# Optimization experiments

Hardware: AMD Instinct MI355X
Metric: run time of the kernel (lower is better)

## Reference

```python
import jax, jax.numpy as jnp
import numpy as np

N_NODES = 50000
N_EDGES = 800000
N_GRAPHS = 128


def gcn_conv(x, row, col, W, b, num_nodes):
    # GCNConv: x' = D^-1/2 (A + I) D^-1/2 (x W) + b, with self-loops added.
    h = x @ W  # [N, out]
    # append self-loops
    sl = jnp.arange(num_nodes, dtype=row.dtype)
    r = jnp.concatenate([row, sl])
    c = jnp.concatenate([col, sl])
    deg = jax.ops.segment_sum(jnp.ones_like(r, dtype=h.dtype), r, num_segments=num_nodes)
    dinv = jnp.where(deg > 0, jax.lax.rsqrt(deg), 0.0)
    norm = dinv[r] * dinv[c]  # [E+N]
    msg = h[c] * norm[:, None]  # gather + scale
    out = jax.ops.segment_sum(msg, r, num_segments=num_nodes)
    return out + b


def setup_inputs() -> dict:
    key = jax.random.key(0)
    k = jax.random.split(key, 6)
    x = jax.random.normal(k[0], (N_NODES, 256), dtype=jnp.float32)
    edge_index = jax.random.randint(k[1], (2, N_EDGES), 0, N_NODES, dtype=jnp.int32)
    batch = jnp.sort(jax.random.randint(k[2], (N_NODES,), 0, N_GRAPHS, dtype=jnp.int32))
    W1 = jax.random.normal(k[3], (256, 128), dtype=jnp.float32) * (1.0 / np.sqrt(256))
    b1 = jnp.zeros((128,), dtype=jnp.float32)
    W2 = jax.random.normal(k[4], (128, 32), dtype=jnp.float32) * (1.0 / np.sqrt(128))
    b2 = jnp.zeros((32,), dtype=jnp.float32)
    return {"x": x, "edge_index": edge_index, "batch": batch,
            "W1": W1, "b1": b1, "W2": W2, "b2": b2}


def reference(x, edge_index, batch, W1, b1, W2, b2):
    row, col = edge_index[0], edge_index[1]
    h = gcn_conv(x, row, col, W1, b1, N_NODES)
    h = jax.nn.relu(h)
    # dropout is identity in eval mode (training=False)
    h = gcn_conv(h, row, col, W2, b2, N_NODES)
    # global_mean_pool over batch ids
    sums = jax.ops.segment_sum(h, batch, num_segments=N_GRAPHS)
    cnts = jax.ops.segment_sum(jnp.ones((N_NODES,), dtype=h.dtype), batch, num_segments=N_GRAPHS)
    pooled = sums / jnp.clip(cnts, 1.0)[:, None]  # [G, num_classes]
    return jax.nn.log_softmax(pooled, axis=1)
```

## Files before the change

kernel.cpp:

```cpp
#include <hip/hip_runtime.h>
#include <hip/hip_bf16.h>
#include <math.h>

#define N_NODES 50000
#define N_EDGES 800000
#define N_GRAPHS 128
#define DIM0 256
#define DIM1 128
#define DIM2 32

#define NBUCK 196
#define NEB 98

using f32x4 = __attribute__((ext_vector_type(4))) float;
using s16x8 = __attribute__((ext_vector_type(8))) short;

__device__ inline unsigned bf16pack(float a, float b) {
    __hip_bfloat162 h2 = __float22bfloat162_rn(make_float2(a, b));
    unsigned r;
    __builtin_memcpy(&r, &h2, 4);
    return r;
}
__device__ inline float2 bf16x2(unsigned p) {
    return make_float2(__uint_as_float(p << 16), __uint_as_float(p & 0xffff0000u));
}

__device__ inline int featOf(int p) {
    return 32 * (p >> 5) + ((p >> 1) & 15) + 16 * (p & 1);
}

__device__ inline void gather16x2(const unsigned* __restrict__ h1u, int ecA, int jA, int ecB, int jB,
                                  int lane, float2& accA, float2& accB) {
    int cA[16], cB[16];
#pragma unroll
    for (int u = 0; u < 16; ++u) cA[u] = __shfl(ecA, jA + u);
#pragma unroll
    for (int u = 0; u < 16; ++u) cB[u] = __shfl(ecB, jB + u);
    unsigned pA[16], pB[16];
#pragma unroll
    for (int u = 0; u < 16; ++u) pA[u] = h1u[(size_t)cA[u] * 64 + lane];
#pragma unroll
    for (int u = 0; u < 16; ++u) pB[u] = h1u[(size_t)cB[u] * 64 + lane];
    float sx = 0.f, sy = 0.f;
#pragma unroll
    for (int u = 0; u < 16; ++u) { float2 v = bf16x2(pA[u]); sx += v.x; sy += v.y; }
    accA.x += sx; accA.y += sy;
    sx = 0.f; sy = 0.f;
#pragma unroll
    for (int u = 0; u < 16; ++u) { float2 v = bf16x2(pB[u]); sx += v.x; sy += v.y; }
    accB.x += sx; accB.y += sy;
}
template <int W>
__device__ inline void gatherW(const unsigned* __restrict__ h1u, int ec, int j, int lane, float2& acc) {
    int c[W];
#pragma unroll
    for (int u = 0; u < W; ++u) c[u] = __shfl(ec, j + u);
    unsigned p[W];
#pragma unroll
    for (int u = 0; u < W; ++u) p[u] = h1u[(size_t)c[u] * 64 + lane];
    float sx = 0.f, sy = 0.f;
#pragma unroll
    for (int u = 0; u < W; ++u) { float2 v = bf16x2(p[u]); sx += v.x; sy += v.y; }
    acc.x += sx; acc.y += sy;
}
__device__ inline void gatherTail(const unsigned* __restrict__ h1u, int ec, int& j, int n, int lane, float2& acc) {
    for (; j + 16 <= n; j += 16) gatherW<16>(h1u, ec, j, lane, acc);
    for (; j + 8 <= n; j += 8) gatherW<8>(h1u, ec, j, lane, acc);
    for (; j + 4 <= n; j += 4) gatherW<4>(h1u, ec, j, lane, acc);
    for (; j < n; ++j) {
        int c = __shfl(ec, j);
        float2 v = bf16x2(h1u[(size_t)c * 64 + lane]);
        acc.x += v.x; acc.y += v.y;
    }
}

__global__ __launch_bounds__(256) void k_hist(const int* __restrict__ row, int* __restrict__ hist) {
    __shared__ int h[NBUCK];
    int b = blockIdx.x, t = threadIdx.x;
    if (t < NBUCK) h[t] = 0;
    __syncthreads();
#pragma unroll
    for (int i = 0; i < 8; ++i) {
        int idx = b * 2048 + i * 256 + t;
        if (idx < N_EDGES / 4) {
            int4 r4 = ((const int4*)row)[idx];
            atomicAdd(&h[r4.x >> 8], 1);
            atomicAdd(&h[r4.y >> 8], 1);
            atomicAdd(&h[r4.z >> 8], 1);
            atomicAdd(&h[r4.w >> 8], 1);
        }
    }
    __syncthreads();
    if (t < NBUCK) hist[b * NBUCK + t] = h[t];
}

__global__ __launch_bounds__(256) void k_place(const int* __restrict__ row, const int* __restrict__ col,
                                               const int* __restrict__ hist, uint* __restrict__ bb,
                                               int* __restrict__ bbase, int* __restrict__ btot,
                                               const float* __restrict__ W1, uint* __restrict__ W1b,
                                               const float* __restrict__ W2, uint* __restrict__ W2b,
                                               const int* __restrict__ batch, int* gstart,
                                               float* __restrict__ pooled) {
    __shared__ int cur[NBUCK];
    __shared__ int tot[NBUCK];
    __shared__ int sc[256];
    int blk = blockIdx.x, t = threadIdx.x;
    if (blk >= NEB) {
        if (blk == NEB + 16) {
            for (int i = t; i < N_GRAPHS * DIM2; i += 256) pooled[i] = 0.f;
            return;
        }
        int g = (blk - NEB) * 256 + t;
        {
            int s = g >> 9, tt = (g >> 6) & 7, q = (g >> 4) & 3, n = g & 15;
            int k0 = s * 32 + q * 8;
            int colw = tt * 16 + n;
            uint4 o;
            o.x = bf16pack(W1[(size_t)(k0 + 0) * DIM1 + colw], W1[(size_t)(k0 + 1) * DIM1 + colw]);
            o.y = bf16pack(W1[(size_t)(k0 + 2) * DIM1 + colw], W1[(size_t)(k0 + 3) * DIM1 + colw]);
            o.z = bf16pack(W1[(size_t)(k0 + 4) * DIM1 + colw], W1[(size_t)(k0 + 5) * DIM1 + colw]);
            o.w = bf16pack(W1[(size_t)(k0 + 6) * DIM1 + colw], W1[(size_t)(k0 + 7) * DIM1 + colw]);
            ((uint4*)W1b)[g] = o;
        }
        if (g < 512) {
            int s = g >> 7, tt = (g >> 6) & 1, l = g & 63;
            int n = tt * 16 + (l & 15);
            int kb = s * 32 + (l >> 4) * 8;
            uint4 o;
            o.x = bf16pack(W2[(size_t)featOf(kb + 0) * DIM2 + n], W2[(size_t)featOf(kb + 1) * DIM2 + n]);
            o.y = bf16pack(W2[(size_t)featOf(kb + 2) * DIM2 + n], W2[(size_t)featOf(kb + 3) * DIM2 + n]);
            o.z = bf16pack(W2[(size_t)featOf(kb + 4) * DIM2 + n], W2[(size_t)featOf(kb + 5) * DIM2 + n]);
            o.w = bf16pack(W2[(size_t)featOf(kb + 6) * DIM2 + n], W2[(size_t)featOf(kb + 7) * DIM2 + n]);
            ((uint4*)W2b)[g] = o;
        }
        if (g <= N_GRAPHS) {
            int lo = 0, hi = N_NODES;
            while (lo < hi) { int mid = (lo + hi) >> 1; if (batch[mid] < g) lo = mid + 1; else hi = mid; }
            gstart[g] = lo;
        }
        return;
    }
    int pre = 0, to = 0;
    for (int b2 = 0; b2 < NEB; ++b2) {
        int v = (t < NBUCK) ? hist[b2 * NBUCK + t] : 0;
        to += v;
        if (b2 < blk) pre += v;
    }
    if (t < NBUCK) tot[t] = to;
    sc[t] = (t < NBUCK) ? to : 0;
    __syncthreads();
    for (int off = 1; off < 256; off <<= 1) {
        int x = (t >= off) ? sc[t - off] : 0;
        __syncthreads();
        sc[t] += x;
        __syncthreads();
    }
    if (t < NBUCK) {
        int base = sc[t] - tot[t];
        cur[t] = base + pre;
        if (blk == 0) { bbase[t] = base; btot[t] = tot[t]; }
    }
    __syncthreads();
#pragma unroll
    for (int i = 0; i < 8; ++i) {
        int idx = blk * 2048 + i * 256 + t;
        if (idx < N_EDGES / 4) {
            int4 r4 = ((const int4*)row)[idx];
            int4 c4 = ((const int4*)col)[idx];
            int rs[4] = {r4.x, r4.y, r4.z, r4.w};
            int cs[4] = {c4.x, c4.y, c4.z, c4.w};
#pragma unroll
            for (int j = 0; j < 4; ++j) {
                int pos = atomicAdd(&cur[rs[j] >> 8], 1);
                bb[pos] = ((uint)(rs[j] & 255) << 16) | (uint)cs[j];
            }
        }
    }
}

__global__ __launch_bounds__(256) void k_build(const int* __restrict__ bbase, const int* __restrict__ btot,
                                               const uint* __restrict__ bb,
                                               int* __restrict__ offs, int* __restrict__ cnt,
                                               ushort* __restrict__ csr) {
    __shared__ int c256[256];
    __shared__ int cur256[256];
    __shared__ int wsum[4];
    int b = blockIdx.x, t = threadIdx.x;
    int start = bbase[b];
    int n = btot[b];
    c256[t] = 0;
    __syncthreads();
    for (int i = t; i < n; i += 256) atomicAdd(&c256[bb[start + i] >> 16], 1);
    __syncthreads();
    int w = t >> 6, l = t & 63;
    int v = c256[t];
    int incl = v;
#pragma unroll
    for (int off = 1; off < 64; off <<= 1) {
        int x = __shfl_up(incl, off, 64);
        if (l >= off) incl += x;
    }
    if (l == 63) wsum[w] = incl;
    __syncthreads();
    int woff = 0;
    for (int i = 0; i < w; ++i) woff += wsum[i];
    int excl = incl - v + woff;
    cur256[t] = excl;
    int r = b * 256 + t;
    if (r < N_NODES) { offs[r] = start + excl; cnt[r] = v; }
    __syncthreads();
    for (int i = t; i < n; i += 256) {
        uint e = bb[start + i];
        int pos = atomicAdd(&cur256[e >> 16], 1);
        csr[start + pos] = (ushort)(e & 0xFFFFu);
    }
}

#define G1_BM 128
#define AS_LD 20
__global__ __launch_bounds__(256) void k_gemm1(const float* __restrict__ X, const uint* __restrict__ W1b,
                                               const int* __restrict__ cnt, unsigned* __restrict__ h1u) {
    __shared__ uint w1s[16384];
    __shared__ uint As[G1_BM * AS_LD];
    int t = threadIdx.x;
    int w = t >> 6, lane = t & 63, q = lane >> 4, m16 = lane & 15;
    int rowBase = blockIdx.x * G1_BM;

    {
        const uint4* src = (const uint4*)W1b;
        uint4* dst = (uint4*)w1s;
#pragma unroll
        for (int i = 0; i < 16; ++i) dst[i * 256 + t] = src[i * 256 + t];
    }

    f32x4 acc[2][8];
#pragma unroll
    for (int i = 0; i < 2; ++i)
#pragma unroll
        for (int j = 0; j < 8; ++j) acc[i][j] = (f32x4){0.f, 0.f, 0.f, 0.f};

    int ar = t >> 1, ah = t & 1;
    for (int s = 0; s < 8; ++s) {
        float4 f0 = {0,0,0,0}, f1 = {0,0,0,0}, f2 = {0,0,0,0}, f3 = {0,0,0,0};
        int grow = rowBase + ar;
        if (grow < N_NODES) {
            const float* src = X + (size_t)grow * DIM0 + s * 32 + ah * 16;
            f0 = *(const float4*)(src + 0);
            f1 = *(const float4*)(src + 4);
            f2 = *(const float4*)(src + 8);
            f3 = *(const float4*)(src + 12);
        }
        uint4 p0, p1;
        p0.x = bf16pack(f0.x, f0.y); p0.y = bf16pack(f0.z, f0.w);
        p0.z = bf16pack(f1.x, f1.y); p0.w = bf16pack(f1.z, f1.w);
        p1.x = bf16pack(f2.x, f2.y); p1.y = bf16pack(f2.z, f2.w);
        p1.z = bf16pack(f3.x, f3.y); p1.w = bf16pack(f3.z, f3.w);
        __syncthreads();
        *(uint4*)&As[ar * AS_LD + ah * 8 + 0] = p0;
        *(uint4*)&As[ar * AS_LD + ah * 8 + 4] = p1;
        __syncthreads();

        s16x8 af[2];
#pragma unroll
        for (int rt = 0; rt < 2; ++rt) {
            int arow = w * 32 + rt * 16 + m16;
            af[rt] = *(s16x8*)&As[arow * AS_LD + q * 4];
        }
#pragma unroll
        for (int tt = 0; tt < 8; ++tt) {
            s16x8 bf = *(s16x8*)&w1s[((s * 8 + tt) * 64 + lane) * 4];
            acc[0][tt] = __builtin_amdgcn_mfma_f32_16x16x32_bf16(af[0], bf, acc[0][tt], 0, 0, 0);
            acc[1][tt] = __builtin_amdgcn_mfma_f32_16x16x32_bf16(af[1], bf, acc[1][tt], 0, 0, 0);
        }
    }

#pragma unroll
    for (int rt = 0; rt < 2; ++rt) {
#pragma unroll
        for (int reg = 0; reg < 4; ++reg) {
            int row = rowBase + w * 32 + rt * 16 + q * 4 + reg;
            if (row < N_NODES) {
                float dv = rsqrtf((float)(cnt[row] + 1));
                unsigned* hr = h1u + (size_t)row * 64;
#pragma unroll
                for (int u = 0; u < 4; ++u)
                    hr[u * 16 + m16] = bf16pack(acc[rt][2 * u][reg] * dv, acc[rt][2 * u + 1][reg] * dv);
            }
        }
    }
}

#define A1_LD 68
__global__ __launch_bounds__(512) void k_agg1g2(const unsigned* __restrict__ h1u, const int* __restrict__ cnt,
                                                const int* __restrict__ offs, const ushort* __restrict__ csr,
                                                const float* __restrict__ b1, const uint* __restrict__ W2b,
                                                unsigned* __restrict__ h2u) {
    __shared__ uint a1tile[16 * A1_LD];
    __shared__ float sdi[16];
    int t = threadIdx.x;
    int wv = t >> 6, lane = t & 63;
    int nb16 = blockIdx.x * 16;

    int mA = wv * 2, mB = wv * 2 + 1;
    int nodeA = nb16 + mA, nodeB = nb16 + mB;
    float2 accA = bf16x2(h1u[(size_t)nodeA * 64 + lane]);
    float2 accB = bf16x2(h1u[(size_t)nodeB * 64 + lane]);
    int nA = cnt[nodeA], nB = cnt[nodeB];
    const ushort* cpA = csr + offs[nodeA];
    const ushort* cpB = csr + offs[nodeB];
    int ecA = (lane < nA) ? cpA[lane] : 0;
    int ecB = (lane < nB) ? cpB[lane] : 0;

    int jA = 0, jB = 0;
    while (jA + 16 <= nA && jB + 16 <= nB) {
        gather16x2(h1u, ecA, jA, ecB, jB, lane, accA, accB);
        jA += 16; jB += 16;
    }
    gatherTail(h1u, ecA, jA, nA, lane, accA);
    gatherTail(h1u, ecB, jB, nB, lane, accB);

    float diA = rsqrtf((float)(nA + 1));
    float diB = rsqrtf((float)(nB + 1));
    if (lane == 0) { sdi[mA] = diA; sdi[mB] = diB; }
    int f0 = (lane >> 4) * 32 + (lane & 15);
    float b1lo = b1[f0], b1hi = b1[f0 + 16];
    accA.x = fmaxf(accA.x * diA + b1lo, 0.f);
    accA.y = fmaxf(accA.y * diA + b1hi, 0.f);
    accB.x = fmaxf(accB.x * diB + b1lo, 0.f);
    accB.y = fmaxf(accB.y * diB + b1hi, 0.f);
    a1tile[mA * A1_LD + lane] = bf16pack(accA.x, accA.y);
    a1tile[mB * A1_LD + lane] = bf16pack(accB.x, accB.y);
    __syncthreads();

    if (wv == 0) {
        int q = lane >> 4, m16 = lane & 15;
        f32x4 accP = (f32x4){0.f, 0.f, 0.f, 0.f};
        f32x4 accQ = (f32x4){0.f, 0.f, 0.f, 0.f};
#pragma unroll
        for (int s = 0; s < 4; ++s) {
            s16x8 af = *(s16x8*)&a1tile[m16 * A1_LD + s * 16 + q * 4];
            s16x8 bf0 = *(const s16x8*)(W2b + (size_t)((s * 2 + 0) * 64 + lane) * 4);
            s16x8 bf1 = *(const s16x8*)(W2b + (size_t)((s * 2 + 1) * 64 + lane) * 4);
            accP = __builtin_amdgcn_mfma_f32_16x16x32_bf16(af, bf0, accP, 0, 0, 0);
            accQ = __builtin_amdgcn_mfma_f32_16x16x32_bf16(af, bf1, accQ, 0, 0, 0);
        }
#pragma unroll
        for (int r = 0; r < 4; ++r) {
            int node = nb16 + q * 4 + r;
            float dv = sdi[q * 4 + r];
            h2u[(size_t)node * 16 + m16] = bf16pack(accP[r] * dv, accQ[r] * dv);
        }
    }
}

__global__ __launch_bounds__(256) void k_agg2pool(const unsigned* __restrict__ h2u, const int* __restrict__ cnt,
                                                  const int* __restrict__ offs, const ushort* __restrict__ csr,
                                                  const int* __restrict__ batch, float* __restrict__ pooled) {
    __shared__ float2 red[16][16];
    int t = threadIdx.x;
    int nb16 = blockIdx.x * 16;
    int node = nb16 + (t >> 4);
    int l = t & 15;
    float2 acc = bf16x2(h2u[(size_t)node * 16 + l]);
    int n = cnt[node];
    const ushort* cp = csr + offs[node];
    for (int base = 0; base < n; base += 16) {
        int m = min(16, n - base);
        int ec = 0;
        if (l < m) ec = cp[base + l];
        int j = 0;
        if (m == 16) {
            int c[16];
#pragma unroll
            for (int u = 0; u < 16; ++u) c[u] = __shfl(ec, u, 16);
            unsigned p[16];
#pragma unroll
            for (int u = 0; u < 16; ++u) p[u] = h2u[(size_t)c[u] * 16 + l];
            float sx = 0.f, sy = 0.f;
#pragma unroll
            for (int u = 0; u < 16; ++u) { float2 v = bf16x2(p[u]); sx += v.x; sy += v.y; }
            acc.x += sx; acc.y += sy;
            j = 16;
        }
        for (; j + 4 <= m; j += 4) {
            int c0 = __shfl(ec, j, 16), c1 = __shfl(ec, j + 1, 16);
            int c2 = __shfl(ec, j + 2, 16), c3 = __shfl(ec, j + 3, 16);
            unsigned p0 = h2u[(size_t)c0 * 16 + l];
            unsigned p1 = h2u[(size_t)c1 * 16 + l];
            unsigned p2 = h2u[(size_t)c2 * 16 + l];
            unsigned p3 = h2u[(size_t)c3 * 16 + l];
            float2 v0 = bf16x2(p0), v1 = bf16x2(p1), v2 = bf16x2(p2), v3 = bf16x2(p3);
            acc.x += v0.x + v1.x + v2.x + v3.x;
            acc.y += v0.y + v1.y + v2.y + v3.y;
        }
        for (; j < m; ++j) {
            int c = __shfl(ec, j, 16);
            float2 v = bf16x2(h2u[(size_t)c * 16 + l]);
            acc.x += v.x; acc.y += v.y;
        }
    }
    float di = rsqrtf((float)(n + 1));
    red[t >> 4][l] = make_float2(acc.x * di, acc.y * di);
    __syncthreads();
    if (t < 16) {
        float2 run = make_float2(0.f, 0.f);
        int gprev = batch[nb16];
        for (int m = 0; m < 16; ++m) {
            int g = batch[nb16 + m];
            if (g != gprev) {
                atomicAdd(&pooled[gprev * DIM2 + t], run.x);
                atomicAdd(&pooled[gprev * DIM2 + t + 16], run.y);
                run = make_float2(0.f, 0.f);
                gprev = g;
            }
            float2 v = red[m][t];
            run.x += v.x; run.y += v.y;
        }
        atomicAdd(&pooled[gprev * DIM2 + t], run.x);
        atomicAdd(&pooled[gprev * DIM2 + t + 16], run.y);
    }
}

__global__ __launch_bounds__(64) void k_final(const float* __restrict__ pooled, const int* __restrict__ gstart,
                                              const float* __restrict__ b2, float* __restrict__ out) {
    int g = blockIdx.x;
    int lane = threadIdx.x;
    float cntf = fmaxf((float)(gstart[g + 1] - gstart[g]), 1.0f);
    float val = 0.f, v = -INFINITY;
    if (lane < DIM2) {
        val = pooled[g * DIM2 + lane] / cntf + b2[lane];
        v = val;
    }
#pragma unroll
    for (int m = 16; m >= 1; m >>= 1) v = fmaxf(v, __shfl_xor(v, m, 32));
    float ex = (lane < DIM2) ? expf(val - v) : 0.f;
#pragma unroll
    for (int m = 16; m >= 1; m >>= 1) ex += __shfl_xor(ex, m, 32);
    if (lane < DIM2) out[g * DIM2 + lane] = val - v - logf(ex);
}

extern "C" void kernel_launch(void* const* d_in, const int* in_sizes, int n_in,
                              void* d_out, int out_size, void* d_ws, size_t ws_size,
                              hipStream_t stream) {
    const float* x     = (const float*)d_in[0];
    const int*   eidx  = (const int*)d_in[1];
    const int*   batch = (const int*)d_in[2];
    const float* W1    = (const float*)d_in[3];
    const float* b1    = (const float*)d_in[4];
    const float* W2    = (const float*)d_in[5];
    const float* b2    = (const float*)d_in[6];
    const int* row = eidx;
    const int* col = eidx + N_EDGES;
    float* out = (float*)d_out;

    char* p = (char*)d_ws;
    int*    cnt    = (int*)p;    p += (size_t)N_NODES * 4;
    int*    offs   = (int*)p;    p += (size_t)N_NODES * 4 + 16;
    int*    gstart = (int*)p;    p += 768;
    uint*   W1b    = (uint*)p;   p += 4096 * 16;
    uint*   W2b    = (uint*)p;   p += 512 * 16;
    int*    hist   = (int*)p;    p += (size_t)NEB * NBUCK * 4 + 32;
    int*    bbase  = (int*)p;    p += 1024;
    int*    btot   = (int*)p;    p += 1024;
    float*  pooled = (float*)p;  p += (size_t)N_GRAPHS * DIM2 * 4;
    uint*   bb     = (uint*)p;   p += (size_t)N_EDGES * 4;
    ushort* csr    = (ushort*)p; p += (size_t)N_EDGES * 2;
    unsigned* h1u  = (unsigned*)p; p += (size_t)N_NODES * 64 * 4;
    unsigned* h2u  = (unsigned*)p; p += (size_t)N_NODES * 16 * 4;

    k_hist<<<NEB, 256, 0, stream>>>(row, hist);
    k_place<<<NEB + 17, 256, 0, stream>>>(row, col, hist, bb, bbase, btot,
                                          W1, W1b, W2, W2b, batch, gstart, pooled);
    k_build<<<NBUCK, 256, 0, stream>>>(bbase, btot, bb, offs, cnt, csr);

    k_gemm1<<<(N_NODES + G1_BM - 1) / G1_BM, 256, 0, stream>>>(x, W1b, cnt, h1u);
    k_agg1g2<<<N_NODES / 16, 512, 0, stream>>>(h1u, cnt, offs, csr, b1, W2b, h2u);
    k_agg2pool<<<N_NODES / 16, 256, 0, stream>>>(h2u, cnt, offs, csr, batch, pooled);
    k_final<<<N_GRAPHS, 64, 0, stream>>>(pooled, gstart, b2, out);
}
```

Baseline: 194.7 us.

## Restructure layer-1 gather into 16-byte vector loads with half-wave node split

```diff
diff --git a/kernel.cpp b/kernel.cpp
--- a/kernel.cpp
+++ b/kernel.cpp
@@ -27,51 +27,6 @@
 
 __device__ inline int featOf(int p) {
     return 32 * (p >> 5) + ((p >> 1) & 15) + 16 * (p & 1);
-}
-
-__device__ inline void gather16x2(const unsigned* __restrict__ h1u, int ecA, int jA, int ecB, int jB,
-                                  int lane, float2& accA, float2& accB) {
-    int cA[16], cB[16];
-#pragma unroll
-    for (int u = 0; u < 16; ++u) cA[u] = __shfl(ecA, jA + u);
-#pragma unroll
-    for (int u = 0; u < 16; ++u) cB[u] = __shfl(ecB, jB + u);
-    unsigned pA[16], pB[16];
-#pragma unroll
-    for (int u = 0; u < 16; ++u) pA[u] = h1u[(size_t)cA[u] * 64 + lane];
-#pragma unroll
-    for (int u = 0; u < 16; ++u) pB[u] = h1u[(size_t)cB[u] * 64 + lane];
-    float sx = 0.f, sy = 0.f;
-#pragma unroll
-    for (int u = 0; u < 16; ++u) { float2 v = bf16x2(pA[u]); sx += v.x; sy += v.y; }
-    accA.x += sx; accA.y += sy;
-    sx = 0.f; sy = 0.f;
-#pragma unroll
-    for (int u = 0; u < 16; ++u) { float2 v = bf16x2(pB[u]); sx += v.x; sy += v.y; }
-    accB.x += sx; accB.y += sy;
-}
-template <int W>
-__device__ inline void gatherW(const unsigned* __restrict__ h1u, int ec, int j, int lane, float2& acc) {
-    int c[W];
-#pragma unroll
-    for (int u = 0; u < W; ++u) c[u] = __shfl(ec, j + u);
-    unsigned p[W];
-#pragma unroll
-    for (int u = 0; u < W; ++u) p[u] = h1u[(size_t)c[u] * 64 + lane];
-    float sx = 0.f, sy = 0.f;
-#pragma unroll
-    for (int u = 0; u < W; ++u) { float2 v = bf16x2(p[u]); sx += v.x; sy += v.y; }
-    acc.x += sx; acc.y += sy;
-}
-__device__ inline void gatherTail(const unsigned* __restrict__ h1u, int ec, int& j, int n, int lane, float2& acc) {
-    for (; j + 16 <= n; j += 16) gatherW<16>(h1u, ec, j, lane, acc);
-    for (; j + 8 <= n; j += 8) gatherW<8>(h1u, ec, j, lane, acc);
-    for (; j + 4 <= n; j += 4) gatherW<4>(h1u, ec, j, lane, acc);
-    for (; j < n; ++j) {
-        int c = __shfl(ec, j);
-        float2 v = bf16x2(h1u[(size_t)c * 64 + lane]);
-        acc.x += v.x; acc.y += v.y;
-    }
 }
 
 __global__ __launch_bounds__(256) void k_hist(const int* __restrict__ row, int* __restrict__ hist) {
@@ -291,45 +246,91 @@
 }
 
 #define A1_LD 68
-__global__ __launch_bounds__(512) void k_agg1g2(const unsigned* __restrict__ h1u, const int* __restrict__ cnt,
-                                                const int* __restrict__ offs, const ushort* __restrict__ csr,
-                                                const float* __restrict__ b1, const uint* __restrict__ W2b,
-                                                unsigned* __restrict__ h2u) {
+__global__ __launch_bounds__(512, 2) void k_agg1g2(const unsigned* __restrict__ h1u, const int* __restrict__ cnt,
+                                                   const int* __restrict__ offs, const ushort* __restrict__ csr,
+                                                   const float* __restrict__ b1, const uint* __restrict__ W2b,
+                                                   unsigned* __restrict__ h2u) {
     __shared__ uint a1tile[16 * A1_LD];
     __shared__ float sdi[16];
     int t = threadIdx.x;
     int wv = t >> 6, lane = t & 63;
+    int grp = lane >> 4, li = lane & 15, sub = grp & 1;
     int nb16 = blockIdx.x * 16;
-
     int mA = wv * 2, mB = wv * 2 + 1;
     int nodeA = nb16 + mA, nodeB = nb16 + mB;
-    float2 accA = bf16x2(h1u[(size_t)nodeA * 64 + lane]);
-    float2 accB = bf16x2(h1u[(size_t)nodeB * 64 + lane]);
     int nA = cnt[nodeA], nB = cnt[nodeB];
     const ushort* cpA = csr + offs[nodeA];
     const ushort* cpB = csr + offs[nodeB];
-    int ecA = (lane < nA) ? cpA[lane] : 0;
-    int ecB = (lane < nB) ? cpB[lane] : 0;
-
-    int jA = 0, jB = 0;
-    while (jA + 16 <= nA && jB + 16 <= nB) {
-        gather16x2(h1u, ecA, jA, ecB, jB, lane, accA, accB);
-        jA += 16; jB += 16;
-    }
-    gatherTail(h1u, ecA, jA, nA, lane, accA);
-    gatherTail(h1u, ecB, jB, nB, lane, accB);
+    int ecA = (lane < nA) ? (int)cpA[lane] : 0;
+    int ecB = (lane < nB) ? (int)cpB[lane] : 0;
+    bool isA = grp < 2;
+    int nSel = isA ? nA : nB;
+    const char* hb = (const char*)h1u;
+
+    float acc[8];
+#pragma unroll
+    for (int u = 0; u < 8; ++u) acc[u] = 0.f;
+
+    auto accum = [&](uint4 v) {
+        float2 a0 = bf16x2(v.x), a1 = bf16x2(v.y), a2 = bf16x2(v.z), a3 = bf16x2(v.w);
+        acc[0] += a0.x; acc[1] += a0.y; acc[2] += a1.x; acc[3] += a1.y;
+        acc[4] += a2.x; acc[5] += a2.y; acc[6] += a3.x; acc[7] += a3.y;
+    };
+    auto fetch = [&](int k) -> uint4 {
+        int item = 2 * k + sub;
+        int cA_ = __shfl(ecA, item);
+        int cB_ = __shfl(ecB, item);
+        int c = isA ? cA_ : cB_;
+        uint4 v = make_uint4(0u, 0u, 0u, 0u);
+        if (item < nSel) {
+            uint off = (uint)c * 256u + (uint)li * 16u;
+            v = *(const uint4*)(hb + off);
+        }
+        return v;
+    };
+
+    if (sub == 0) {
+        int selfNode = isA ? nodeA : nodeB;
+        uint off = (uint)selfNode * 256u + (uint)li * 16u;
+        accum(*(const uint4*)(hb + off));
+    }
+
+    int KK = (max(nA, nB) + 1) >> 1;
+    for (int k = 0; k < KK; k += 4) {
+        uint4 v0 = fetch(k);
+        uint4 v1 = fetch(k + 1);
+        uint4 v2 = fetch(k + 2);
+        uint4 v3 = fetch(k + 3);
+        accum(v0); accum(v1); accum(v2); accum(v3);
+    }
+
+#pragma unroll
+    for (int u = 0; u < 8; ++u) acc[u] += __shfl_xor(acc[u], 16);
 
     float diA = rsqrtf((float)(nA + 1));
     float diB = rsqrtf((float)(nB + 1));
-    if (lane == 0) { sdi[mA] = diA; sdi[mB] = diB; }
-    int f0 = (lane >> 4) * 32 + (lane & 15);
-    float b1lo = b1[f0], b1hi = b1[f0 + 16];
-    accA.x = fmaxf(accA.x * diA + b1lo, 0.f);
-    accA.y = fmaxf(accA.y * diA + b1hi, 0.f);
-    accB.x = fmaxf(accB.x * diB + b1lo, 0.f);
-    accB.y = fmaxf(accB.y * diB + b1hi, 0.f);
-    a1tile[mA * A1_LD + lane] = bf16pack(accA.x, accA.y);
-    a1tile[mB * A1_LD + lane] = bf16pack(accB.x, accB.y);
+    if (lane == 0) sdi[mA] = diA;
+    if (lane == 32) sdi[mB] = diB;
+    float di = isA ? diA : diB;
+    int m = isA ? mA : mB;
+
+    uint o0, o1, o2, o3;
+    {
+        int p = li * 4;
+        int flo0 = 32 * (p >> 4) + (p & 15);
+        float lo, hi;
+        lo = fmaxf(acc[0] * di + b1[flo0 + 0], 0.f);  hi = fmaxf(acc[1] * di + b1[flo0 + 16], 0.f);
+        o0 = bf16pack(lo, hi);
+        lo = fmaxf(acc[2] * di + b1[flo0 + 1], 0.f);  hi = fmaxf(acc[3] * di + b1[flo0 + 17], 0.f);
+        o1 = bf16pack(lo, hi);
+        lo = fmaxf(acc[4] * di + b1[flo0 + 2], 0.f);  hi = fmaxf(acc[5] * di + b1[flo0 + 18], 0.f);
+        o2 = bf16pack(lo, hi);
+        lo = fmaxf(acc[6] * di + b1[flo0 + 3], 0.f);  hi = fmaxf(acc[7] * di + b1[flo0 + 19], 0.f);
+        o3 = bf16pack(lo, hi);
+    }
+    if (sub == 0) {
+        *(uint4*)&a1tile[m * A1_LD + li * 4] = make_uint4(o0, o1, o2, o3);
+    }
     __syncthreads();
 
     if (wv == 0) {
```

Measured after the change: 189.3 us. 1.03x faster.
